# Kernel optimization log

Hardware: AMD Instinct MI355X
Metric: run time of the kernel (lower is better)

Reference implementation:

```python
import jax, jax.numpy as jnp
import numpy as np

EPS = 1e-6

def _ln(x, g, b):
    m = x.mean(-1, keepdims=True)
    v = jnp.var(x, axis=-1, keepdims=True)
    return (x - m) * jax.lax.rsqrt(v + EPS) * g + b

def _mha(x, qkv_w, out_w, out_b, heads, dh):
    # vit-style attention: Linear(dim, 3*heads*dh, bias=False), chunk into q,k,v
    B, N, _ = x.shape
    qkv = (x @ qkv_w).reshape(B, N, 3, heads, dh).transpose(2, 0, 3, 1, 4)
    q, k, v = qkv[0], qkv[1], qkv[2]                       # [B,H,N,dh]
    attn = jax.nn.softmax(jnp.einsum('bhid,bhjd->bhij', q, k) * (dh ** -0.5), axis=-1)
    o = jnp.einsum('bhij,bhjd->bhid', attn, v).transpose(0, 2, 1, 3).reshape(B, N, heads * dh)
    return o @ out_w + out_b

def _tx(x, p, heads, dh):
    # standard prenorm transformer stack, p = stacked per-layer params
    (l1g, l1b, qw, ow, ob, l2g, l2b, f1w, f1b, f2w, f2b, ng, nb) = p
    for i in range(l1g.shape[0]):
        x = x + _mha(_ln(x, l1g[i], l1b[i]), qw[i], ow[i], ob[i], heads, dh)
        h = _ln(x, l2g[i], l2b[i])
        x = x + jax.nn.gelu(h @ f1w[i] + f1b[i]) @ f2w[i] + f2b[i]
    return _ln(x, ng, nb)

def _ats(x, l1g, l1b, qkvw, qkvb, projw, projb, l2g, l2b, f1w, f1b, f2w, f2b):
    # ATS block: attention + CLS-significance-driven adaptive token resampling (gather)
    B, N, D = x.shape
    heads = 6
    dh = D // heads
    h = _ln(x, l1g, l1b)
    qkv = (h @ qkvw + qkvb).reshape(B, N, 3, heads, dh).transpose(2, 0, 3, 1, 4)
    q, k, v = qkv[0], qkv[1], qkv[2]
    attn = jax.nn.softmax(jnp.einsum('bhid,bhjd->bhij', q, k) * (dh ** -0.5), axis=-1)  # [B,H,N,N]
    y = jnp.einsum('bhij,bhjd->bhid', attn, v).transpose(0, 2, 1, 3).reshape(B, N, D)
    y = y @ projw + projb
    # significance score: cls attention * value norm (ATS, Fayyaz et al.)
    vn = jnp.linalg.norm(v, axis=-1)                        # [B,H,N]
    s = (attn[:, :, 0, 1:] * vn[:, :, 1:]).mean(axis=1)     # [B,N-1]
    s = s / (s.sum(-1, keepdims=True) + 1e-8)
    cdf = jnp.cumsum(s, axis=-1)                            # [B,N-1]
    # deterministic inverse-transform sampling of N-1 tokens
    u = (jnp.arange(N - 1, dtype=x.dtype) + 0.5) / (N - 1)
    idx = jax.vmap(lambda c: jnp.searchsorted(c, u))(cdf)
    idx = jnp.clip(idx, 0, N - 2) + 1                       # skip cls slot
    idx = jnp.concatenate([jnp.zeros((B, 1), idx.dtype), idx], axis=1)  # keep cls
    g = lambda a: jnp.take_along_axis(a, idx[:, :, None], axis=1)
    x = g(x) + g(y)
    h = _ln(x, l2g, l2b)
    return x + jax.nn.gelu(h @ f1w + f1b) @ f2w + f2b

def reference(x, patch_w, patch_b, pos_emb, space_token, temporal_token,
              s_ln1_g, s_ln1_b, s_qkv_w, s_out_w, s_out_b, s_ln2_g, s_ln2_b,
              s_fc1_w, s_fc1_b, s_fc2_w, s_fc2_b, s_norm_g, s_norm_b,
              t_ln1_g, t_ln1_b, t_qkv_w, t_out_w, t_out_b, t_ln2_g, t_ln2_b,
              t_fc1_w, t_fc1_b, t_fc2_w, t_fc2_b, t_norm_g, t_norm_b,
              a_ln1_g, a_ln1_b, a_qkv_w, a_qkv_b, a_proj_w, a_proj_b,
              a_ln2_g, a_ln2_b, a_fc1_w, a_fc1_b, a_fc2_w, a_fc2_b,
              final_g, final_b, h1_w, h1_b, h2_w, h2_b):
    B, T = x.shape[0], x.shape[1]
    BT, D, P, HP = B * T, 192, 16, 14
    # patch embedding (conv16s16 as unfold + linear), channel-major flattening
    xt = x.reshape(BT, 3, HP, P, HP, P).transpose(0, 2, 4, 1, 3, 5).reshape(BT, HP * HP, 3 * P * P)
    xt = (xt @ patch_w + patch_b).reshape(B, T, HP * HP, D)
    cls = jnp.broadcast_to(space_token.reshape(1, 1, 1, D), (B, T, 1, D))
    xt = jnp.concatenate([cls, xt], axis=2) + pos_emb      # [B,T,197,D]
    xt = xt.reshape(BT, 197, D)
    xt = _tx(xt, (s_ln1_g, s_ln1_b, s_qkv_w, s_out_w, s_out_b, s_ln2_g, s_ln2_b,
                  s_fc1_w, s_fc1_b, s_fc2_w, s_fc2_b, s_norm_g, s_norm_b), 6, 64)
    for i in range(a_ln1_g.shape[0]):
        xt = _ats(xt, a_ln1_g[i], a_ln1_b[i], a_qkv_w[i], a_qkv_b[i], a_proj_w[i],
                  a_proj_b[i], a_ln2_g[i], a_ln2_b[i], a_fc1_w[i], a_fc1_b[i],
                  a_fc2_w[i], a_fc2_b[i])
    xc = xt[:, 0].reshape(B, T, D)
    tt = jnp.broadcast_to(temporal_token, (B, 1, D))
    xc = jnp.concatenate([tt, xc], axis=1)                 # [B,T+1,D]
    xc = _tx(xc, (t_ln1_g, t_ln1_b, t_qkv_w, t_out_w, t_out_b, t_ln2_g, t_ln2_b,
                  t_fc1_w, t_fc1_b, t_fc2_w, t_fc2_b, t_norm_g, t_norm_b), 6, 64)
    f = jnp.max(xc, axis=1)                                # AdaptiveMaxPool1d(1) over tokens
    f = _ln(f, final_g, final_b)
    return jax.nn.relu(f @ h1_w + h1_b) @ h2_w + h2_b      # mlp_head -> [B,2]

def setup_inputs():
    key = jax.random.key(0)
    ks = iter(jax.random.split(key, 64))
    def rn(shape, s=0.02):
        return jax.random.normal(next(ks), shape, dtype=jnp.float32) * s
    d = {}
    d['x'] = jax.random.normal(next(ks), (16, 5, 3, 224, 224), dtype=jnp.float32)
    d['patch_w'] = rn((768, 192)); d['patch_b'] = jnp.zeros((192,), jnp.float32)
    d['pos_emb'] = rn((1, 5, 197, 192))
    d['space_token'] = rn((1, 1, 192)); d['temporal_token'] = rn((1, 1, 192))
    def tx(depth, n):
        d[n + '_ln1_g'] = jnp.ones((depth, 192), jnp.float32); d[n + '_ln1_b'] = jnp.zeros((depth, 192), jnp.float32)
        d[n + '_qkv_w'] = rn((depth, 192, 1152)); d[n + '_out_w'] = rn((depth, 384, 192)); d[n + '_out_b'] = jnp.zeros((depth, 192), jnp.float32)
        d[n + '_ln2_g'] = jnp.ones((depth, 192), jnp.float32); d[n + '_ln2_b'] = jnp.zeros((depth, 192), jnp.float32)
        d[n + '_fc1_w'] = rn((depth, 192, 768)); d[n + '_fc1_b'] = jnp.zeros((depth, 768), jnp.float32)
        d[n + '_fc2_w'] = rn((depth, 768, 192)); d[n + '_fc2_b'] = jnp.zeros((depth, 192), jnp.float32)
        d[n + '_norm_g'] = jnp.ones((192,), jnp.float32); d[n + '_norm_b'] = jnp.zeros((192,), jnp.float32)
    tx(2, 's'); tx(3, 't')
    d['a_ln1_g'] = jnp.ones((12, 192), jnp.float32); d['a_ln1_b'] = jnp.zeros((12, 192), jnp.float32)
    d['a_qkv_w'] = rn((12, 192, 576)); d['a_qkv_b'] = jnp.zeros((12, 576), jnp.float32)
    d['a_proj_w'] = rn((12, 192, 192)); d['a_proj_b'] = jnp.zeros((12, 192), jnp.float32)
    d['a_ln2_g'] = jnp.ones((12, 192), jnp.float32); d['a_ln2_b'] = jnp.zeros((12, 192), jnp.float32)
    d['a_fc1_w'] = rn((12, 192, 768)); d['a_fc1_b'] = jnp.zeros((12, 768), jnp.float32)
    d['a_fc2_w'] = rn((12, 768, 192)); d['a_fc2_b'] = jnp.zeros((12, 192), jnp.float32)
    d['final_g'] = jnp.ones((192,), jnp.float32); d['final_b'] = jnp.zeros((192,), jnp.float32)
    d['h1_w'] = rn((192, 64)); d['h1_b'] = jnp.zeros((64,), jnp.float32)
    d['h2_w'] = rn((64, 2)); d['h2_b'] = jnp.zeros((2,), jnp.float32)
    return d
```

## Files before the change

### kernel.cpp

```cpp
#include <hip/hip_runtime.h>
#include <hip/hip_bf16.h>
#include <math.h>

typedef float in_t;
typedef float out_t;

__device__ __forceinline__ float ldi(const in_t* p, size_t i) { return (float)p[i]; }

#define DMODEL 192
#define NTOK   197
#define BT_    80
#define ROWS_  (BT_*NTOK)

__device__ __forceinline__ float gelu_f(float v) {
  return 0.5f*v*(1.f + tanhf(0.7978845608028654f*(v + 0.044715f*v*v*v)));
}

__device__ __forceinline__ short f2bf(float f) {
  union { float f; unsigned u; } v; v.f = f;
  unsigned r = v.u + 0x7FFFu + ((v.u >> 16) & 1u);
  return (short)(r >> 16);
}

typedef __attribute__((ext_vector_type(8))) short bfrag;
typedef __attribute__((ext_vector_type(4))) float f32x4;

__global__ __launch_bounds__(256)
void wconv_k(const float* __restrict__ W, short* __restrict__ O, int K, int N)
{
  __shared__ float tile[32][33];
  const int l = blockIdx.z;
  const int k0 = blockIdx.y*32, n0 = blockIdx.x*32;
  const float* Wl = W + (size_t)l*K*N;
  short* Ol = O + (size_t)l*K*N;
  const int tx = threadIdx.x & 31, ty = threadIdx.x >> 5;
  #pragma unroll
  for (int r = ty; r < 32; r += 8) {
    int k = k0 + r, n = n0 + tx;
    tile[r][tx] = (k < K && n < N) ? Wl[(size_t)k*N + n] : 0.f;
  }
  __syncthreads();
  #pragma unroll
  for (int r = ty; r < 32; r += 8) {
    int n = n0 + r, k = k0 + tx;
    if (n < N && k < K) Ol[(size_t)n*K + k] = f2bf(tile[tx][r]);
  }
}

template<int EPI, int ABF, int OBF>
__global__ __launch_bounds__(256)
void gemmW_k(const void* __restrict__ Ain, const short* __restrict__ Wt,
             const float* __restrict__ bias, const float* __restrict__ R,
             void* __restrict__ Cout, float* __restrict__ Cout2,
             int M, int N, int K)
{
  constexpr int LP = 200;
  __shared__ short Asb[64][LP];
  __shared__ short Bsb[64][LP];
  const int t = threadIdx.x;
  const int w = t >> 6, lane = t & 63;
  const int bm0 = blockIdx.y*64, bn0 = blockIdx.x*64;
  const int sr = t >> 2;
  const int sk = (t & 3) * 8;
  f32x4 acc[4] = {};

  for (int k0 = 0; k0 < K; k0 += 192) {
    const int gm = bm0 + sr;
    #pragma unroll
    for (int cc = 0; cc < 6; ++cc) {
      const int kk = cc*32 + sk;
      short y[8] = {0,0,0,0,0,0,0,0};
      if (gm < M) {
        if (ABF == 0) {
          const float* ap = (const float*)Ain + (size_t)gm*K + k0 + kk;
          float4 v0 = *(const float4*)ap;
          float4 v1 = *(const float4*)(ap + 4);
          y[0]=f2bf(v0.x); y[1]=f2bf(v0.y); y[2]=f2bf(v0.z); y[3]=f2bf(v0.w);
          y[4]=f2bf(v1.x); y[5]=f2bf(v1.y); y[6]=f2bf(v1.z); y[7]=f2bf(v1.w);
        } else {
          *(bfrag*)y = *(const bfrag*)((const short*)Ain + (size_t)gm*K + k0 + kk);
        }
      }
      *(bfrag*)&Asb[sr][kk] = *(bfrag*)y;
      bfrag bv = *(const bfrag*)(Wt + (size_t)(bn0 + sr)*K + k0 + kk);
      *(bfrag*)&Bsb[sr][kk] = bv;
    }
    __syncthreads();
    const int fr = lane & 15, g8 = (lane >> 4) * 8;
    #pragma unroll
    for (int ks = 0; ks < 6; ++ks) {
      bfrag af = *(const bfrag*)&Asb[w*16 + fr][ks*32 + g8];
      #pragma unroll
      for (int nt = 0; nt < 4; ++nt) {
        bfrag bf = *(const bfrag*)&Bsb[nt*16 + fr][ks*32 + g8];
        acc[nt] = __builtin_amdgcn_mfma_f32_16x16x32_bf16(af, bf, acc[nt], 0, 0, 0);
      }
    }
    __syncthreads();
  }
  const int col = lane & 15, rg = (lane >> 4) * 4;
  #pragma unroll
  for (int nt = 0; nt < 4; ++nt) {
    int gn = bn0 + nt*16 + col;
    float bv = bias ? bias[gn] : 0.f;
    #pragma unroll
    for (int r = 0; r < 4; ++r) {
      int gm = bm0 + w*16 + rg + r;
      if (gm < M) {
        float v = acc[nt][r] + bv;
        if (EPI==1) v = gelu_f(v);
        if (EPI==2) v += R[(size_t)gm*N + gn];
        if (OBF==0)      ((float*)Cout)[(size_t)gm*N + gn] = v;
        else if (OBF==1) ((short*)Cout)[(size_t)gm*N + gn] = f2bf(v);
        else {
          if (gn < 384) ((short*)Cout)[(size_t)gm*384 + gn] = f2bf(v);
          else          Cout2[(size_t)gm*192 + (gn - 384)] = v;
        }
      }
    }
  }
}

__global__ __launch_bounds__(256)
void ffn_k(const float* __restrict__ Ain, const short* __restrict__ W1t,
           const float* __restrict__ b1, const short* __restrict__ W2t,
           const float* __restrict__ b2, const float* __restrict__ R,
           float* __restrict__ Cout, int M)
{
  constexpr int LP = 200, FP = 776;
  __shared__ short As[64][LP];
  __shared__ short Bs[64][LP];
  __shared__ short FF[64][FP];
  const int t = threadIdx.x;
  const int w = t >> 6, lane = t & 63;
  const int bm0 = blockIdx.x*64;
  const int sr = t >> 2;
  const int sk = (t & 3) * 8;
  const int fr = lane & 15, g8 = (lane >> 4) * 8;
  const int col = lane & 15, rg = (lane >> 4) * 4;

  {
    const int gm = bm0 + sr;
    #pragma unroll
    for (int cc = 0; cc < 6; ++cc) {
      const int kk = cc*32 + sk;
      short y[8] = {0,0,0,0,0,0,0,0};
      if (gm < M) {
        const float* ap = Ain + (size_t)gm*192 + kk;
        float4 v0 = *(const float4*)ap;
        float4 v1 = *(const float4*)(ap + 4);
        y[0]=f2bf(v0.x); y[1]=f2bf(v0.y); y[2]=f2bf(v0.z); y[3]=f2bf(v0.w);
        y[4]=f2bf(v1.x); y[5]=f2bf(v1.y); y[6]=f2bf(v1.z); y[7]=f2bf(v1.w);
      }
      *(bfrag*)&As[sr][kk] = *(bfrag*)y;
    }
  }
  for (int nc = 0; nc < 12; ++nc) {
    #pragma unroll
    for (int cc = 0; cc < 6; ++cc) {
      const int kk = cc*32 + sk;
      bfrag bv = *(const bfrag*)(W1t + (size_t)(nc*64 + sr)*192 + kk);
      *(bfrag*)&Bs[sr][kk] = bv;
    }
    __syncthreads();
    f32x4 acc[4] = {};
    #pragma unroll
    for (int ks = 0; ks < 6; ++ks) {
      bfrag af = *(const bfrag*)&As[w*16 + fr][ks*32 + g8];
      #pragma unroll
      for (int nt = 0; nt < 4; ++nt) {
        bfrag bf = *(const bfrag*)&Bs[nt*16 + fr][ks*32 + g8];
        acc[nt] = __builtin_amdgcn_mfma_f32_16x16x32_bf16(af, bf, acc[nt], 0, 0, 0);
      }
    }
    #pragma unroll
    for (int nt = 0; nt < 4; ++nt) {
      int gn = nc*64 + nt*16 + col;
      float bv = b1[gn];
      #pragma unroll
      for (int r = 0; r < 4; ++r)
        FF[w*16 + rg + r][gn] = f2bf(gelu_f(acc[nt][r] + bv));
    }
    __syncthreads();
  }
  for (int nc = 0; nc < 3; ++nc) {
    f32x4 acc[4] = {};
    for (int kc = 0; kc < 4; ++kc) {
      #pragma unroll
      for (int cc = 0; cc < 6; ++cc) {
        const int kk = cc*32 + sk;
        bfrag bv = *(const bfrag*)(W2t + (size_t)(nc*64 + sr)*768 + kc*192 + kk);
        *(bfrag*)&Bs[sr][kk] = bv;
      }
      __syncthreads();
      #pragma unroll
      for (int ks = 0; ks < 6; ++ks) {
        bfrag af = *(const bfrag*)&FF[w*16 + fr][kc*192 + ks*32 + g8];
        #pragma unroll
        for (int nt = 0; nt < 4; ++nt) {
          bfrag bf = *(const bfrag*)&Bs[nt*16 + fr][ks*32 + g8];
          acc[nt] = __builtin_amdgcn_mfma_f32_16x16x32_bf16(af, bf, acc[nt], 0, 0, 0);
        }
      }
      __syncthreads();
    }
    #pragma unroll
    for (int nt = 0; nt < 4; ++nt) {
      int gn = nc*64 + nt*16 + col;
      float bv = b2[gn];
      #pragma unroll
      for (int r = 0; r < 4; ++r) {
        int gm = bm0 + w*16 + rg + r;
        if (gm < M) {
          float v = acc[nt][r] + bv + R[(size_t)gm*192 + gn];
          Cout[(size_t)gm*192 + gn] = v;
        }
      }
    }
  }
}

__global__ __launch_bounds__(256)
void ln_k(const float* __restrict__ x, const in_t* __restrict__ g, const in_t* __restrict__ b,
          float* __restrict__ o, int rows)
{
  int t = threadIdx.x, wave = t>>6, lane = t&63;
  int r = blockIdx.x*4 + wave;
  if (r >= rows) return;
  const float* xr = x + (size_t)r*DMODEL;
  float e0 = xr[lane], e1 = xr[lane+64], e2 = xr[lane+128];
  float s = e0+e1+e2;
  #pragma unroll
  for (int off=32; off; off>>=1) s += __shfl_xor(s, off);
  float mean = s / 192.f;
  float d0=e0-mean, d1=e1-mean, d2=e2-mean;
  float v = d0*d0+d1*d1+d2*d2;
  #pragma unroll
  for (int off=32; off; off>>=1) v += __shfl_xor(v, off);
  float rs = 1.f / sqrtf(v/192.f + 1e-6f);
  float* orow = o + (size_t)r*DMODEL;
  orow[lane]     = d0*rs*ldi(g,lane)     + ldi(b,lane);
  orow[lane+64]  = d1*rs*ldi(g,lane+64)  + ldi(b,lane+64);
  orow[lane+128] = d2*rs*ldi(g,lane+128) + ldi(b,lane+128);
}

__global__ __launch_bounds__(256)
void gatherln_k(const float* __restrict__ X, const float* __restrict__ P,
                const int* __restrict__ idx, const in_t* __restrict__ g,
                const in_t* __restrict__ b, float* __restrict__ Xo,
                float* __restrict__ H2, int rows)
{
  int t = threadIdx.x, wave = t>>6, lane = t&63;
  int r = blockIdx.x*4 + wave;
  if (r >= rows) return;
  int bt = r / NTOK, n = r - bt*NTOK;
  int src = idx[(size_t)bt*NTOK + n];
  size_t sb = ((size_t)bt*NTOK + src)*DMODEL;
  float e0 = X[sb+lane]     + P[sb+lane];
  float e1 = X[sb+lane+64]  + P[sb+lane+64];
  float e2 = X[sb+lane+128] + P[sb+lane+128];
  float* xr = Xo + (size_t)r*DMODEL;
  xr[lane] = e0; xr[lane+64] = e1; xr[lane+128] = e2;
  float s = e0+e1+e2;
  #pragma unroll
  for (int off=32; off; off>>=1) s += __shfl_xor(s, off);
  float mean = s / 192.f;
  float d0=e0-mean, d1=e1-mean, d2=e2-mean;
  float v = d0*d0+d1*d1+d2*d2;
  #pragma unroll
  for (int off=32; off; off>>=1) v += __shfl_xor(v, off);
  float rs = 1.f / sqrtf(v/192.f + 1e-6f);
  float* orow = H2 + (size_t)r*DMODEL;
  orow[lane]     = d0*rs*ldi(g,lane)     + ldi(b,lane);
  orow[lane+64]  = d1*rs*ldi(g,lane+64)  + ldi(b,lane+64);
  orow[lane+128] = d2*rs*ldi(g,lane+128) + ldi(b,lane+128);
}

template<int DH, int W, int MODE>
__global__ __launch_bounds__(W*64)
void attnB_k(const short* __restrict__ qk, const float* __restrict__ vf,
             short* __restrict__ out, float* __restrict__ attn0,
             int heads, float scale)
{
  constexpr int NSEQ = 197;
  constexpr int NP   = 224;
  constexpr int KG   = DH/8;
  constexpr int CT   = DH/16;
  constexpr int NF   = DH/32;
  __shared__ short Kb[KG][NP][8];
  __shared__ short Vt[NP/8][DH][8];
  __shared__ short Ps[W][NP/8][16][8];

  const int bh = blockIdx.x;
  const int b = bh / heads, h = bh - b*heads;
  const int qks = ((MODE==1) ? 3 : 2)*heads*DH;
  const short* __restrict__ baseqk = qk + (size_t)b*NSEQ*qks;
  const int qo = h*DH, ko = heads*DH + h*DH;
  const int vs = heads*DH;
  const float* __restrict__ basev = (MODE==2) ? (vf + (size_t)b*NSEQ*vs) : nullptr;
  const int vo = (MODE==1) ? (2*heads*DH + h*DH) : (h*DH);
  const int t = threadIdx.x, w = t>>6, lane = t&63;

  {
    short z8[8] = {0,0,0,0,0,0,0,0};
    for (int idx = t; idx < NP*KG; idx += W*64) {
      int j = idx / KG, dg = idx - j*KG;
      bfrag kv = *(bfrag*)z8;
      if (j < NSEQ) kv = *(const bfrag*)(baseqk + (size_t)j*qks + ko + dg*8);
      *(bfrag*)&Kb[dg][j][0] = kv;
    }
  }
  for (int idx = t; idx < NP*DH; idx += W*64) {
    int j = idx / DH, d = idx - j*DH;
    short vv = 0;
    if (j < NSEQ) {
      if (MODE==1) vv = baseqk[(size_t)j*qks + vo + d];
      else         vv = f2bf(basev[(size_t)j*vs + vo + d]);
    }
    Vt[j>>3][d][j&7] = vv;
  }
  __syncthreads();

  const int c = lane & 15, g = lane >> 4, rg = g*4;
  const float NEG = -3.0e38f;

  for (int st = w; st < 13; st += W) {
    const int q0 = st*16;
    int qrow = q0 + c; if (qrow > NSEQ-1) qrow = NSEQ-1;
    bfrag aq[NF];
    {
      const short* qp = baseqk + (size_t)qrow*qks + qo + g*8;
      #pragma unroll
      for (int f = 0; f < NF; ++f) aq[f] = *(const bfrag*)(qp + f*32);
    }
    f32x4 sacc[14];
    #pragma unroll
    for (int jt = 0; jt < 14; ++jt) sacc[jt] = (f32x4){0.f,0.f,0.f,0.f};
    #pragma unroll
    for (int jt = 0; jt < 13; ++jt) {
      #pragma unroll
      for (int f = 0; f < NF; ++f) {
        bfrag bk = *(const bfrag*)&Kb[f*4 + g][jt*16 + c][0];
        sacc[jt] = __builtin_amdgcn_mfma_f32_16x16x32_bf16(aq[f], bk, sacc[jt], 0, 0, 0);
      }
    }
    float m0[4] = {NEG,NEG,NEG,NEG};
    #pragma unroll
    for (int jt = 0; jt < 14; ++jt) {
      const bool valid = (jt < 13) && (jt*16 + c < NSEQ);
      #pragma unroll
      for (int r = 0; r < 4; ++r) {
        float sv = valid ? sacc[jt][r]*scale : NEG;
        sacc[jt][r] = sv;
        m0[r] = fmaxf(m0[r], sv);
      }
    }
    #pragma unroll
    for (int off = 1; off < 16; off <<= 1)
      #pragma unroll
      for (int r = 0; r < 4; ++r) m0[r] = fmaxf(m0[r], __shfl_xor(m0[r], off));
    float sum[4] = {0.f,0.f,0.f,0.f};
    #pragma unroll
    for (int jt = 0; jt < 14; ++jt)
      #pragma unroll
      for (int r = 0; r < 4; ++r) {
        float e = expf(sacc[jt][r] - m0[r]);
        sacc[jt][r] = e;
        sum[r] += e;
      }
    #pragma unroll
    for (int off = 1; off < 16; off <<= 1)
      #pragma unroll
      for (int r = 0; r < 4; ++r) sum[r] += __shfl_xor(sum[r], off);
    float inv[4];
    #pragma unroll
    for (int r = 0; r < 4; ++r) inv[r] = 1.f / sum[r];

    if (attn0 != nullptr && st == 0 && g == 0) {
      #pragma unroll
      for (int jt = 0; jt < 13; ++jt) {
        int j = jt*16 + c;
        if (j < NSEQ) attn0[(size_t)bh*NSEQ + j] = sacc[jt][0]*inv[0];
      }
    }
    #pragma unroll
    for (int jt = 0; jt < 14; ++jt)
      #pragma unroll
      for (int r = 0; r < 4; ++r)
        Ps[w][jt*2 + (c>>3)][rg + r][c&7] = f2bf(sacc[jt][r]);
    f32x4 oacc[CT];
    #pragma unroll
    for (int ct = 0; ct < CT; ++ct) oacc[ct] = (f32x4){0.f,0.f,0.f,0.f};
    #pragma unroll
    for (int kc = 0; kc < 7; ++kc) {
      bfrag ap = *(const bfrag*)&Ps[w][kc*4 + g][c][0];
      #pragma unroll
      for (int ct = 0; ct < CT; ++ct) {
        bfrag bv = *(const bfrag*)&Vt[kc*4 + g][ct*16 + c][0];
        oacc[ct] = __builtin_amdgcn_mfma_f32_16x16x32_bf16(ap, bv, oacc[ct], 0, 0, 0);
      }
    }
    #pragma unroll
    for (int ct = 0; ct < CT; ++ct)
      #pragma unroll
      for (int r = 0; r < 4; ++r) {
        int q = q0 + rg + r;
        if (q < NSEQ)
          out[((size_t)b*NSEQ + q)*(size_t)(heads*DH) + h*DH + ct*16 + c] = f2bf(oacc[ct][r]*inv[r]);
      }
  }
}

template<int DH, int W>
__global__ __launch_bounds__(W*64)
void attn2r_k(const float* __restrict__ qkv, float* __restrict__ out,
              float* __restrict__ attn0, int Nseq, int heads, float scale)
{
  constexpr int QT = 8;
  constexpr int KTS = 204;
  constexpr int NPART = (DH == 64) ? 1 : 2;
  constexpr int DQ   = DH/4;
  constexpr int QPG  = 2;
  __shared__ float Kt[DH * KTS];
  __shared__ float Qt[W][DH][12];
  __shared__ float Ps[W][QT][200];

  const int bh = blockIdx.x;
  const int b = bh / heads, h = bh % heads;
  const int stride = 3 * heads * DH;
  const float* __restrict__ base = qkv + (size_t)b * Nseq * stride;
  const int qo = h * DH, ko = heads * DH + h * DH, vo = 2 * heads * DH + h * DH;
  const int t = threadIdx.x, w = t >> 6, lane = t & 63;

  for (int idx = t; idx < Nseq * DH; idx += W * 64) {
    int j = idx / DH, d0 = idx - j * DH;
    Kt[d0 * KTS + j] = base[(size_t)j * stride + ko + d0];
  }
  __syncthreads();

  const int d = lane & (DH - 1);
  const int nchunks = (Nseq + QT - 1) / QT;
  const int jcmax = (Nseq + 3) >> 2;
  const float NEG = -3.0e38f;
  const float4* Kt4 = (const float4*)Kt;

  const int part = (NPART == 2) ? (lane >> 5) : 0;
  const int qg   = (DH == 64) ? (lane >> 4) : ((lane >> 3) & 3);
  const int dq   = lane & (DQ - 1);
  const int dv   = 4 * dq;

  for (int ic = w; ic < nchunks; ic += W) {
    const int i0 = ic * QT;
    if ((DH == 64) || (lane >> 5) == 0) {
      #pragma unroll
      for (int q = 0; q < QT; ++q) {
        int i = i0 + q;
        Qt[w][d][q] = (i < Nseq) ? base[(size_t)i * stride + qo + d] : 0.f;
      }
    }
    float s[QT][4];
    #pragma unroll
    for (int q = 0; q < QT; ++q)
      #pragma unroll
      for (int u = 0; u < 4; ++u) s[q][u] = 0.f;
    #pragma unroll 4
    for (int dd = 0; dd < DH; ++dd) {
      float4 kv = (lane < 51) ? Kt4[dd * (KTS/4) + lane] : make_float4(0.f,0.f,0.f,0.f);
      float4 qA = *(const float4*)&Qt[w][dd][0];
      float4 qB = *(const float4*)&Qt[w][dd][4];
      float qv[8] = {qA.x, qA.y, qA.z, qA.w, qB.x, qB.y, qB.z, qB.w};
      float kr[4] = {kv.x, kv.y, kv.z, kv.w};
      #pragma unroll
      for (int q = 0; q < QT; ++q)
        #pragma unroll
        for (int u = 0; u < 4; ++u)
          s[q][u] = fmaf(qv[q], kr[u], s[q][u]);
    }
    float inv[QT];
    #pragma unroll
    for (int q = 0; q < QT; ++q) {
      float mx = NEG;
      #pragma unroll
      for (int u = 0; u < 4; ++u) {
        int j = 4*lane + u;
        s[q][u] = (j < Nseq) ? s[q][u]*scale : NEG;
        mx = fmaxf(mx, s[q][u]);
      }
      #pragma unroll
      for (int off = 32; off; off >>= 1) mx = fmaxf(mx, __shfl_xor(mx, off));
      float sum = 0.f;
      #pragma unroll
      for (int u = 0; u < 4; ++u) {
        float p = (4*lane + u < Nseq) ? expf(s[q][u] - mx) : 0.f;
        s[q][u] = p; sum += p;
      }
      #pragma unroll
      for (int off = 32; off; off >>= 1) sum += __shfl_xor(sum, off);
      inv[q] = 1.f / sum;
      if (lane < 50)
        *(float4*)&Ps[w][q][4*lane] = make_float4(s[q][0], s[q][1], s[q][2], s[q][3]);
    }
    if (attn0 != nullptr && i0 == 0) {
      #pragma unroll
      for (int u = 0; u < 4; ++u) {
        int j = 4*lane + u;
        if (j < Nseq) attn0[(size_t)bh*Nseq + j] = s[0][u]*inv[0];
      }
    }
    float o[QPG][4];
    #pragma unroll
    for (int qi = 0; qi < QPG; ++qi) { o[qi][0]=0.f; o[qi][1]=0.f; o[qi][2]=0.f; o[qi][3]=0.f; }
    const float* __restrict__ Vg = base + vo;
    for (int jc = part; jc < jcmax; jc += NPART) {
      const int jb = 4*jc;
      float4 V0 = make_float4(0.f,0.f,0.f,0.f), V1=V0, V2=V0, V3=V0;
      if (jb+0 < Nseq) V0 = *(const float4*)&Vg[(size_t)(jb+0)*stride + dv];
      if (jb+1 < Nseq) V1 = *(const float4*)&Vg[(size_t)(jb+1)*stride + dv];
      if (jb+2 < Nseq) V2 = *(const float4*)&Vg[(size_t)(jb+2)*stride + dv];
      if (jb+3 < Nseq) V3 = *(const float4*)&Vg[(size_t)(jb+3)*stride + dv];
      #pragma unroll
      for (int qi = 0; qi < QPG; ++qi) {
        float4 p4 = *(const float4*)&Ps[w][qg*QPG+qi][jb];
        o[qi][0] = fmaf(p4.w,V3.x, fmaf(p4.z,V2.x, fmaf(p4.y,V1.x, fmaf(p4.x,V0.x, o[qi][0]))));
        o[qi][1] = fmaf(p4.w,V3.y, fmaf(p4.z,V2.y, fmaf(p4.y,V1.y, fmaf(p4.x,V0.y, o[qi][1]))));
        o[qi][2] = fmaf(p4.w,V3.z, fmaf(p4.z,V2.z, fmaf(p4.y,V1.z, fmaf(p4.x,V0.z, o[qi][2]))));
        o[qi][3] = fmaf(p4.w,V3.w, fmaf(p4.z,V2.w, fmaf(p4.y,V1.w, fmaf(p4.x,V0.w, o[qi][3]))));
      }
    }
    if (NPART == 2) {
      #pragma unroll
      for (int qi = 0; qi < QPG; ++qi) {
        o[qi][0] += __shfl_xor(o[qi][0], 32);
        o[qi][1] += __shfl_xor(o[qi][1], 32);
        o[qi][2] += __shfl_xor(o[qi][2], 32);
        o[qi][3] += __shfl_xor(o[qi][3], 32);
      }
    }
    if (part == 0) {
      #pragma unroll
      for (int qi = 0; qi < QPG; ++qi) {
        float iv = inv[qi];
        if (qg == 1) iv = inv[QPG + qi];
        if (qg == 2) iv = inv[2*QPG + qi];
        if (qg == 3) iv = inv[3*QPG + qi];
        int i = i0 + qg*QPG + qi;
        if (i < Nseq) {
          float4 r = make_float4(o[qi][0]*iv, o[qi][1]*iv, o[qi][2]*iv, o[qi][3]*iv);
          *(float4*)&out[((size_t)b*Nseq + i)*(size_t)(heads*DH) + h*DH + dv] = r;
        }
      }
    }
  }
}

__global__ void patchify_k(const in_t* __restrict__ x, short* __restrict__ A)
{
  int idx = blockIdx.x*256 + threadIdx.x;
  const int total = BT_*196*768;
  if (idx >= total) return;
  int kc = idx % 768;
  int m  = idx / 768;
  int p  = m % 196;
  int bt = m / 196;
  int c  = kc >> 8;
  int py = (kc >> 4) & 15;
  int px = kc & 15;
  int ph = p / 14, pw = p % 14;
  size_t src = (((size_t)bt*3 + c)*224 + (ph*16+py))*224 + (pw*16+px);
  A[idx] = f2bf(ldi(x, src));
}

__global__ void assemble_k(const float* __restrict__ pt, const in_t* __restrict__ st,
                           const in_t* __restrict__ pe, float* __restrict__ X)
{
  int i = blockIdx.x*256 + threadIdx.x;
  const int total = BT_*NTOK*DMODEL;
  if (i >= total) return;
  int d  = i % DMODEL;
  int n  = (i / DMODEL) % NTOK;
  int bt = i / (DMODEL*NTOK);
  int tt = bt % 5;
  float base = (n == 0) ? ldi(st, d)
                        : pt[((size_t)bt*196 + (n-1))*DMODEL + d];
  X[i] = base + ldi(pe, ((size_t)tt*NTOK + n)*DMODEL + d);
}

__global__ __launch_bounds__(256)
void scoresample_k(const float* __restrict__ attn0, const float* __restrict__ Vf,
                   int* __restrict__ idxout)
{
  __shared__ float S[196];
  __shared__ float cdf[196];
  int b = blockIdx.x, t = threadIdx.x;
  if (t < 196) {
    int j = t + 1;
    float acc = 0.f;
    #pragma unroll
    for (int h = 0; h < 6; ++h) {
      float a0 = attn0[((size_t)b*6 + h)*NTOK + j];
      const float* v = Vf + ((size_t)b*NTOK + j)*192 + h*32;
      float ss = 0.f;
      #pragma unroll
      for (int d = 0; d < 32; ++d) ss += v[d]*v[d];
      acc += a0 * sqrtf(ss);
    }
    S[t] = acc / 6.0f;
  }
  __syncthreads();
  if (t == 0) {
    float tot = 0.f;
    for (int k = 0; k < 196; ++k) tot += S[k];
    float denom = tot + 1e-8f;
    float run = 0.f;
    for (int k = 0; k < 196; ++k) { run += S[k] / denom; cdf[k] = run; }
    idxout[(size_t)b*NTOK] = 0;
  }
  __syncthreads();
  if (t < 196) {
    float u = ((float)t + 0.5f) / 196.0f;
    int cnt = 0;
    for (int k = 0; k < 196; ++k) cnt += (cdf[k] < u) ? 1 : 0;
    int c = cnt > 195 ? 195 : cnt;
    idxout[(size_t)b*NTOK + 1 + t] = c + 1;
  }
}

__global__ void build_xc_k(const float* __restrict__ X, const in_t* __restrict__ tt,
                           float* __restrict__ xc)
{
  int i = blockIdx.x*256 + threadIdx.x;
  const int total = 16*6*DMODEL;
  if (i >= total) return;
  int d = i % DMODEL;
  int n = (i / DMODEL) % 6;
  int b = i / (DMODEL*6);
  xc[i] = (n == 0) ? ldi(tt, d)
                   : X[(((size_t)b*5 + (n-1))*NTOK + 0)*DMODEL + d];
}

__global__ __launch_bounds__(256)
void head_k(const float* __restrict__ xc, const in_t* __restrict__ fg, const in_t* __restrict__ fb,
            const in_t* __restrict__ w1, const in_t* __restrict__ b1,
            const in_t* __restrict__ w2, const in_t* __restrict__ b2,
            out_t* __restrict__ outp)
{
  __shared__ float fn[DMODEL];
  __shared__ float hid[64];
  __shared__ float mv[2];
  int b = blockIdx.x, t = threadIdx.x;
  if (t < DMODEL) {
    float m = xc[((size_t)b*6 + 0)*DMODEL + t];
    #pragma unroll
    for (int n = 1; n < 6; ++n) m = fmaxf(m, xc[((size_t)b*6 + n)*DMODEL + t]);
    fn[t] = m;
  }
  __syncthreads();
  if (t == 0) {
    float s = 0.f;
    for (int d = 0; d < DMODEL; ++d) s += fn[d];
    float mean = s / 192.f;
    float v = 0.f;
    for (int d = 0; d < DMODEL; ++d) { float dd = fn[d]-mean; v += dd*dd; }
    mv[0] = mean; mv[1] = 1.f / sqrtf(v/192.f + 1e-6f);
  }
  __syncthreads();
  if (t < DMODEL) fn[t] = (fn[t]-mv[0])*mv[1]*ldi(fg,t) + ldi(fb,t);
  __syncthreads();
  if (t < 64) {
    float a = ldi(b1, t);
    for (int d = 0; d < DMODEL; ++d) a += fn[d]*ldi(w1, (size_t)d*64 + t);
    hid[t] = fmaxf(a, 0.f);
  }
  __syncthreads();
  if (t < 2) {
    float a = ldi(b2, t);
    for (int j = 0; j < 64; ++j) a += hid[j]*ldi(w2, (size_t)j*2 + t);
    outp[(size_t)b*2 + t] = (out_t)a;
  }
}

extern "C" void kernel_launch(void* const* d_in, const int* in_sizes, int n_in,
                              void* d_out, int out_size, void* d_ws, size_t ws_size,
                              hipStream_t stream)
{
  if (n_in < 50) return;
  const in_t* x_in     = (const in_t*)d_in[0];
  const in_t* patch_w  = (const in_t*)d_in[1];
  const in_t* patch_b  = (const in_t*)d_in[2];
  const in_t* pos_emb  = (const in_t*)d_in[3];
  const in_t* space_tk = (const in_t*)d_in[4];
  const in_t* temp_tk  = (const in_t*)d_in[5];
  const in_t* s_ln1_g = (const in_t*)d_in[6];  const in_t* s_ln1_b = (const in_t*)d_in[7];
  const in_t* s_qkv_w = (const in_t*)d_in[8];  const in_t* s_out_w = (const in_t*)d_in[9];
  const in_t* s_out_b = (const in_t*)d_in[10]; const in_t* s_ln2_g = (const in_t*)d_in[11];
  const in_t* s_ln2_b = (const in_t*)d_in[12]; const in_t* s_fc1_w = (const in_t*)d_in[13];
  const in_t* s_fc1_b = (const in_t*)d_in[14]; const in_t* s_fc2_w = (const in_t*)d_in[15];
  const in_t* s_fc2_b = (const in_t*)d_in[16]; const in_t* s_nrm_g = (const in_t*)d_in[17];
  const in_t* s_nrm_b = (const in_t*)d_in[18];
  const in_t* t_ln1_g = (const in_t*)d_in[19]; const in_t* t_ln1_b = (const in_t*)d_in[20];
  const in_t* t_qkv_w = (const in_t*)d_in[21]; const in_t* t_out_w = (const in_t*)d_in[22];
  const in_t* t_out_b = (const in_t*)d_in[23]; const in_t* t_ln2_g = (const in_t*)d_in[24];
  const in_t* t_ln2_b = (const in_t*)d_in[25]; const in_t* t_fc1_w = (const in_t*)d_in[26];
  const in_t* t_fc1_b = (const in_t*)d_in[27]; const in_t* t_fc2_w = (const in_t*)d_in[28];
  const in_t* t_fc2_b = (const in_t*)d_in[29]; const in_t* t_nrm_g = (const in_t*)d_in[30];
  const in_t* t_nrm_b = (const in_t*)d_in[31];
  const in_t* a_ln1_g = (const in_t*)d_in[32]; const in_t* a_ln1_b = (const in_t*)d_in[33];
  const in_t* a_qkv_w = (const in_t*)d_in[34]; const in_t* a_qkv_b = (const in_t*)d_in[35];
  const in_t* a_prj_w = (const in_t*)d_in[36]; const in_t* a_prj_b = (const in_t*)d_in[37];
  const in_t* a_ln2_g = (const in_t*)d_in[38]; const in_t* a_ln2_b = (const in_t*)d_in[39];
  const in_t* a_fc1_w = (const in_t*)d_in[40]; const in_t* a_fc1_b = (const in_t*)d_in[41];
  const in_t* a_fc2_w = (const in_t*)d_in[42]; const in_t* a_fc2_b = (const in_t*)d_in[43];
  const in_t* final_g = (const in_t*)d_in[44]; const in_t* final_b = (const in_t*)d_in[45];
  const in_t* h1_w = (const in_t*)d_in[46];    const in_t* h1_b = (const in_t*)d_in[47];
  const in_t* h2_w = (const in_t*)d_in[48];    const in_t* h2_b = (const in_t*)d_in[49];

  float* ws = (float*)d_ws;
  size_t off = 0;
  auto alloc = [&](size_t nf) { size_t r = off; off += (nf + 63) & ~((size_t)63); return r; };
  size_t oX    = alloc((size_t)ROWS_*DMODEL);
  size_t oX2   = alloc((size_t)ROWS_*DMODEL);
  size_t oH    = alloc((size_t)ROWS_*DMODEL);
  size_t oH2   = alloc((size_t)ROWS_*DMODEL);
  size_t oY    = alloc((size_t)ROWS_*384);
  size_t oVf   = alloc((size_t)ROWS_*192);
  size_t oA0   = alloc((size_t)480*NTOK);
  size_t oXC   = alloc((size_t)16*6*DMODEL);
  size_t oIDX  = alloc((size_t)BT_*NTOK);
  size_t oQKVt = alloc((size_t)96*1152);
  size_t oFFt  = alloc((size_t)96*768);
  size_t oWB   = alloc((size_t)4202496 + 64);
  size_t oQKVb = alloc((size_t)ROWS_*1152/2 + 64);
  size_t oYb   = alloc((size_t)ROWS_*384/2 + 64);
  size_t oFFb  = alloc((size_t)ROWS_*768/2 + 64);
  if (ws_size < off*sizeof(float)) return;

  float* X    = ws + oX;
  float* X2   = ws + oX2;
  float* H    = ws + oH;
  float* H2   = ws + oH2;
  float* Y    = ws + oY;
  float* Vf   = ws + oVf;
  float* A0   = ws + oA0;
  float* XC   = ws + oXC;
  int*   IDX  = (int*)(ws + oIDX);
  float* QKVt = ws + oQKVt;
  float* FFt  = ws + oFFt;
  short* WB   = (short*)(ws + oWB);
  short* QKVb = (short*)(ws + oQKVb);
  short* Yb   = (short*)(ws + oYb);
  short* FFb  = (short*)(ws + oFFb);

  size_t wo = 0;
  auto wslot = [&](size_t n){ size_t r = wo; wo += n; return r; };
  size_t wPatch = wslot(147456);
  size_t wSqkv  = wslot(442368);
  size_t wSout  = wslot(147456);
  size_t wSfc1  = wslot(294912);
  size_t wSfc2  = wslot(294912);
  size_t wAqkv  = wslot(1327104);
  size_t wAprj  = wslot(442368);
  size_t wAfc1  = wslot(1769472);
  size_t wAfc2  = wslot(1769472);
  size_t wTqkv  = wslot(663552);
  size_t wTout  = wslot(221184);
  size_t wTfc1  = wslot(442368);
  size_t wTfc2  = wslot(442368);

  auto wconv = [&](const in_t* W, size_t slot, int K, int N, int L) {
    dim3 g(N/32, K/32, L);
    hipLaunchKernelGGL(wconv_k, g, dim3(256), 0, stream, W, WB + slot, K, N);
  };
  wconv(patch_w, wPatch, 768, 192, 1);
  wconv(s_qkv_w, wSqkv, 192, 1152, 2);
  wconv(s_out_w, wSout, 384, 192, 2);
  wconv(s_fc1_w, wSfc1, 192, 768, 2);
  wconv(s_fc2_w, wSfc2, 768, 192, 2);
  wconv(a_qkv_w, wAqkv, 192, 576, 12);
  wconv(a_prj_w, wAprj, 192, 192, 12);
  wconv(a_fc1_w, wAfc1, 192, 768, 12);
  wconv(a_fc2_w, wAfc2, 768, 192, 12);
  wconv(t_qkv_w, wTqkv, 192, 1152, 3);
  wconv(t_out_w, wTout, 384, 192, 3);
  wconv(t_fc1_w, wTfc1, 192, 768, 3);
  wconv(t_fc2_w, wTfc2, 768, 192, 3);

  auto gemm = [&](int epi, int abf, int obf, const void* A, const short* Wt,
                  const float* bias, const float* R, void* C, float* C2,
                  int M, int N, int K) {
    dim3 grid(N/64, (M+63)/64);
    if (obf==2)                        hipLaunchKernelGGL((gemmW_k<0,0,2>), grid, dim3(256), 0, stream, A, Wt, bias, R, C, C2, M, N, K);
    else if (epi==0 && abf==0 && obf==0) hipLaunchKernelGGL((gemmW_k<0,0,0>), grid, dim3(256), 0, stream, A, Wt, bias, R, C, C2, M, N, K);
    else if (epi==0 && abf==0 && obf==1) hipLaunchKernelGGL((gemmW_k<0,0,1>), grid, dim3(256), 0, stream, A, Wt, bias, R, C, C2, M, N, K);
    else if (epi==0 && abf==1 && obf==0) hipLaunchKernelGGL((gemmW_k<0,1,0>), grid, dim3(256), 0, stream, A, Wt, bias, R, C, C2, M, N, K);
    else if (epi==1 && obf==1)         hipLaunchKernelGGL((gemmW_k<1,0,1>), grid, dim3(256), 0, stream, A, Wt, bias, R, C, C2, M, N, K);
    else if (epi==1)                   hipLaunchKernelGGL((gemmW_k<1,0,0>), grid, dim3(256), 0, stream, A, Wt, bias, R, C, C2, M, N, K);
    else if (epi==2 && abf==1)         hipLaunchKernelGGL((gemmW_k<2,1,0>), grid, dim3(256), 0, stream, A, Wt, bias, R, C, C2, M, N, K);
    else                               hipLaunchKernelGGL((gemmW_k<2,0,0>), grid, dim3(256), 0, stream, A, Wt, bias, R, C, C2, M, N, K);
  };
  auto ln = [&](const float* xi, const in_t* g, const in_t* b, float* o, int rows) {
    hipLaunchKernelGGL(ln_k, dim3((rows+3)/4), dim3(256), 0, stream, xi, g, b, o, rows);
  };
  auto ffn = [&](const float* A, size_t w1, const float* b1, size_t w2, const float* b2,
                 const float* R, float* C, int M) {
    hipLaunchKernelGGL(ffn_k, dim3((M+63)/64), dim3(256), 0, stream,
                       A, WB + w1, b1, WB + w2, b2, R, C, M);
  };

  {
    int total = BT_*196*768;
    hipLaunchKernelGGL(patchify_k, dim3((total+255)/256), dim3(256), 0, stream, x_in, FFb);
    gemm(0, 1, 0, FFb, WB + wPatch, patch_b, nullptr, Y, nullptr, 15680, 192, 768);
    int tot2 = BT_*NTOK*DMODEL;
    hipLaunchKernelGGL(assemble_k, dim3((tot2+255)/256), dim3(256), 0, stream, Y, space_tk, pos_emb, X);
  }

  const float sc64 = 0.125f;
  const float sc32 = 0.17677669529663687f;

  for (int i = 0; i < 2; ++i) {
    ln(X, s_ln1_g + (size_t)i*192, s_ln1_b + (size_t)i*192, H, ROWS_);
    gemm(0, 0, 1, H, WB + wSqkv + (size_t)i*192*1152, nullptr, nullptr, QKVb, nullptr, ROWS_, 1152, 192);
    hipLaunchKernelGGL((attnB_k<64,8,1>), dim3(BT_*6), dim3(512), 0, stream, QKVb, (const float*)nullptr, Yb, (float*)nullptr, 6, sc64);
    gemm(2, 1, 0, Yb, WB + wSout + (size_t)i*384*192, s_out_b + (size_t)i*192, X, X, nullptr, ROWS_, 192, 384);
    ln(X, s_ln2_g + (size_t)i*192, s_ln2_b + (size_t)i*192, H, ROWS_);
    ffn(H, wSfc1 + (size_t)i*192*768, s_fc1_b + (size_t)i*768,
        wSfc2 + (size_t)i*768*192, s_fc2_b + (size_t)i*192, X, X, ROWS_);
  }
  ln(X, s_nrm_g, s_nrm_b, X, ROWS_);

  float* xa = X; float* xb = X2;
  for (int i = 0; i < 12; ++i) {
    ln(xa, a_ln1_g + (size_t)i*192, a_ln1_b + (size_t)i*192, H, ROWS_);
    gemm(0, 0, 2, H, WB + wAqkv + (size_t)i*192*576, a_qkv_b + (size_t)i*576, nullptr, QKVb, Vf, ROWS_, 576, 192);
    hipLaunchKernelGGL((attnB_k<32,4,2>), dim3(BT_*6), dim3(256), 0, stream, QKVb, Vf, Yb, A0, 6, sc32);
    gemm(0, 1, 0, Yb, WB + wAprj + (size_t)i*192*192, a_prj_b + (size_t)i*192, nullptr, H, nullptr, ROWS_, 192, 192);
    hipLaunchKernelGGL(scoresample_k, dim3(BT_), dim3(256), 0, stream, A0, Vf, IDX);
    hipLaunchKernelGGL(gatherln_k, dim3((ROWS_+3)/4), dim3(256), 0, stream,
                       xa, H, IDX, a_ln2_g + (size_t)i*192, a_ln2_b + (size_t)i*192, xb, H2, ROWS_);
    ffn(H2, wAfc1 + (size_t)i*192*768, a_fc1_b + (size_t)i*768,
        wAfc2 + (size_t)i*768*192, a_fc2_b + (size_t)i*192, xb, xb, ROWS_);
    float* tmp = xa; xa = xb; xb = tmp;
  }

  {
    int tot = 16*6*DMODEL;
    hipLaunchKernelGGL(build_xc_k, dim3((tot+255)/256), dim3(256), 0, stream, xa, temp_tk, XC);
  }
  const int MT = 16*6;
  for (int i = 0; i < 3; ++i) {
    ln(XC, t_ln1_g + (size_t)i*192, t_ln1_b + (size_t)i*192, H, MT);
    gemm(0, 0, 0, H, WB + wTqkv + (size_t)i*192*1152, nullptr, nullptr, QKVt, nullptr, MT, 1152, 192);
    hipLaunchKernelGGL((attn2r_k<64,8>), dim3(16*6), dim3(512), 0, stream, QKVt, Y, (float*)nullptr, 6, 6, sc64);
    gemm(2, 0, 0, Y, WB + wTout + (size_t)i*384*192, t_out_b + (size_t)i*192, XC, XC, nullptr, MT, 192, 384);
    ln(XC, t_ln2_g + (size_t)i*192, t_ln2_b + (size_t)i*192, H, MT);
    gemm(1, 0, 0, H, WB + wTfc1 + (size_t)i*192*768, t_fc1_b + (size_t)i*768, nullptr, FFt, nullptr, MT, 768, 192);
    gemm(2, 0, 0, FFt, WB + wTfc2 + (size_t)i*768*192, t_fc2_b + (size_t)i*192, XC, XC, nullptr, MT, 192, 768);
  }
  ln(XC, t_nrm_g, t_nrm_b, XC, MT);

  hipLaunchKernelGGL(head_k, dim3(16), dim3(256), 0, stream, XC, final_g, final_b,
                     h1_w, h1_b, h2_w, h2_b, (out_t*)d_out);
}
```

Before: 2.663 ms.

## Stream FFN weights from global and split hidden buffer to cut LDS

The fused FFN kernel no longer stages weight tiles in shared memory. Each wave loads W1/W2 fragments directly from global memory and works only on its own 16 rows, which removes most block barriers. The GELU hidden buffer is processed in two halves, with fc2 partial sums kept in 12 register accumulators, roughly halving LDS use so more blocks can be resident. The trade-offs are uncoalesced, cache-dependent global weight loads per MFMA and higher register pressure.

```diff
diff --git a/kernel.cpp b/kernel.cpp
--- a/kernel.cpp
+++ b/kernel.cpp
@@ -127,10 +127,8 @@
            const float* __restrict__ b2, const float* __restrict__ R,
            float* __restrict__ Cout, int M)
 {
-  constexpr int LP = 200, FP = 776;
-  __shared__ short As[64][LP];
-  __shared__ short Bs[64][LP];
-  __shared__ short FF[64][FP];
+  __shared__ short As[64][200];
+  __shared__ short FF[64][392];
   const int t = threadIdx.x;
   const int w = t >> 6, lane = t & 63;
   const int bm0 = blockIdx.x*64;
@@ -138,6 +136,7 @@
   const int sk = (t & 3) * 8;
   const int fr = lane & 15, g8 = (lane >> 4) * 8;
   const int col = lane & 15, rg = (lane >> 4) * 4;
+  const int row = w*16 + fr;
 
   {
     const int gm = bm0 + sr;
@@ -155,66 +154,56 @@
       *(bfrag*)&As[sr][kk] = *(bfrag*)y;
     }
   }
-  for (int nc = 0; nc < 12; ++nc) {
-    #pragma unroll
-    for (int cc = 0; cc < 6; ++cc) {
-      const int kk = cc*32 + sk;
-      bfrag bv = *(const bfrag*)(W1t + (size_t)(nc*64 + sr)*192 + kk);
-      *(bfrag*)&Bs[sr][kk] = bv;
-    }
-    __syncthreads();
-    f32x4 acc[4] = {};
-    #pragma unroll
-    for (int ks = 0; ks < 6; ++ks) {
-      bfrag af = *(const bfrag*)&As[w*16 + fr][ks*32 + g8];
-      #pragma unroll
-      for (int nt = 0; nt < 4; ++nt) {
-        bfrag bf = *(const bfrag*)&Bs[nt*16 + fr][ks*32 + g8];
-        acc[nt] = __builtin_amdgcn_mfma_f32_16x16x32_bf16(af, bf, acc[nt], 0, 0, 0);
-      }
-    }
-    #pragma unroll
-    for (int nt = 0; nt < 4; ++nt) {
-      int gn = nc*64 + nt*16 + col;
-      float bv = b1[gn];
-      #pragma unroll
-      for (int r = 0; r < 4; ++r)
-        FF[w*16 + rg + r][gn] = f2bf(gelu_f(acc[nt][r] + bv));
-    }
-    __syncthreads();
-  }
-  for (int nc = 0; nc < 3; ++nc) {
-    f32x4 acc[4] = {};
-    for (int kc = 0; kc < 4; ++kc) {
-      #pragma unroll
-      for (int cc = 0; cc < 6; ++cc) {
-        const int kk = cc*32 + sk;
-        bfrag bv = *(const bfrag*)(W2t + (size_t)(nc*64 + sr)*768 + kc*192 + kk);
-        *(bfrag*)&Bs[sr][kk] = bv;
-      }
-      __syncthreads();
+  __syncthreads();
+
+  f32x4 acc2[12] = {};
+
+  #pragma unroll
+  for (int half = 0; half < 2; ++half) {
+    for (int nc6 = 0; nc6 < 6; ++nc6) {
+      const int nc = half*6 + nc6;
+      f32x4 a1[4] = {};
       #pragma unroll
       for (int ks = 0; ks < 6; ++ks) {
-        bfrag af = *(const bfrag*)&FF[w*16 + fr][kc*192 + ks*32 + g8];
+        bfrag af = *(const bfrag*)&As[row][ks*32 + g8];
         #pragma unroll
         for (int nt = 0; nt < 4; ++nt) {
-          bfrag bf = *(const bfrag*)&Bs[nt*16 + fr][ks*32 + g8];
-          acc[nt] = __builtin_amdgcn_mfma_f32_16x16x32_bf16(af, bf, acc[nt], 0, 0, 0);
+          bfrag bf = *(const bfrag*)(W1t + (size_t)(nc*64 + nt*16 + fr)*192 + ks*32 + g8);
+          a1[nt] = __builtin_amdgcn_mfma_f32_16x16x32_bf16(af, bf, a1[nt], 0, 0, 0);
         }
       }
-      __syncthreads();
-    }
-    #pragma unroll
-    for (int nt = 0; nt < 4; ++nt) {
-      int gn = nc*64 + nt*16 + col;
-      float bv = b2[gn];
-      #pragma unroll
-      for (int r = 0; r < 4; ++r) {
-        int gm = bm0 + w*16 + rg + r;
-        if (gm < M) {
-          float v = acc[nt][r] + bv + R[(size_t)gm*192 + gn];
-          Cout[(size_t)gm*192 + gn] = v;
+      #pragma unroll
+      for (int nt = 0; nt < 4; ++nt) {
+        int gn = nc*64 + nt*16 + col;
+        float bv = b1[gn];
+        #pragma unroll
+        for (int r = 0; r < 4; ++r)
+          FF[w*16 + rg + r][nc6*64 + nt*16 + col] = f2bf(gelu_f(a1[nt][r] + bv));
+      }
+    }
+    #pragma unroll
+    for (int kcl = 0; kcl < 2; ++kcl) {
+      #pragma unroll
+      for (int ks = 0; ks < 6; ++ks) {
+        bfrag af = *(const bfrag*)&FF[row][kcl*192 + ks*32 + g8];
+        #pragma unroll
+        for (int nt = 0; nt < 12; ++nt) {
+          bfrag bf = *(const bfrag*)(W2t + (size_t)(nt*16 + fr)*768 + (half*2 + kcl)*192 + ks*32 + g8);
+          acc2[nt] = __builtin_amdgcn_mfma_f32_16x16x32_bf16(af, bf, acc2[nt], 0, 0, 0);
         }
+      }
+    }
+  }
+  #pragma unroll
+  for (int nt = 0; nt < 12; ++nt) {
+    int gn = nt*16 + col;
+    float bv = b2[gn];
+    #pragma unroll
+    for (int r = 0; r < 4; ++r) {
+      int gm = bm0 + w*16 + rg + r;
+      if (gm < M) {
+        float v = acc2[nt][r] + bv + R[(size_t)gm*192 + gn];
+        Cout[(size_t)gm*192 + gn] = v;
       }
     }
   }
```

Measured after the change: 3.416 ms. 28.2% more time.

## Use 8 waves in fused FFN kernel, splitting N tiles across wave pairs

Applied to the files above, without the earlier changes.

The fused FFN kernel goes from 4 to 8 waves per block. Each row band of 16 is now shared by two waves that each compute half of the 64-column tile. The second GEMM loop is reordered to keep all 6 output accumulators live across the K chunks, so the FF tile is reused. A missing barrier after the A-tile staging is also added. The aim is more latency hiding and more MFMA parallelism per block, at the cost of more threads contending for the same LDS and barriers.

```diff
diff --git a/kernel.cpp b/kernel.cpp
--- a/kernel.cpp
+++ b/kernel.cpp
@@ -121,29 +121,30 @@
   }
 }
 
-__global__ __launch_bounds__(256)
+__global__ __launch_bounds__(512)
 void ffn_k(const float* __restrict__ Ain, const short* __restrict__ W1t,
            const float* __restrict__ b1, const short* __restrict__ W2t,
            const float* __restrict__ b2, const float* __restrict__ R,
            float* __restrict__ Cout, int M)
 {
-  constexpr int LP = 200, FP = 776;
-  __shared__ short As[64][LP];
-  __shared__ short Bs[64][LP];
-  __shared__ short FF[64][FP];
+  __shared__ short As[64][200];
+  __shared__ short Bs[64][200];
+  __shared__ short FF[64][776];
   const int t = threadIdx.x;
   const int w = t >> 6, lane = t & 63;
   const int bm0 = blockIdx.x*64;
-  const int sr = t >> 2;
-  const int sk = (t & 3) * 8;
+  const int sr = t >> 3;
+  const int sk8 = (t & 7) * 8;
   const int fr = lane & 15, g8 = (lane >> 4) * 8;
   const int col = lane & 15, rg = (lane >> 4) * 4;
+  const int band = w & 3, nh = w >> 2;
+  const int row = band*16 + fr;
 
   {
     const int gm = bm0 + sr;
     #pragma unroll
-    for (int cc = 0; cc < 6; ++cc) {
-      const int kk = cc*32 + sk;
+    for (int cc = 0; cc < 3; ++cc) {
+      const int kk = cc*64 + sk8;
       short y[8] = {0,0,0,0,0,0,0,0};
       if (gm < M) {
         const float* ap = Ain + (size_t)gm*192 + kk;
@@ -155,64 +156,70 @@
       *(bfrag*)&As[sr][kk] = *(bfrag*)y;
     }
   }
+  __syncthreads();
+
   for (int nc = 0; nc < 12; ++nc) {
     #pragma unroll
-    for (int cc = 0; cc < 6; ++cc) {
-      const int kk = cc*32 + sk;
+    for (int cc = 0; cc < 3; ++cc) {
+      const int kk = cc*64 + sk8;
       bfrag bv = *(const bfrag*)(W1t + (size_t)(nc*64 + sr)*192 + kk);
       *(bfrag*)&Bs[sr][kk] = bv;
     }
     __syncthreads();
-    f32x4 acc[4] = {};
+    f32x4 a1[2] = {};
     #pragma unroll
     for (int ks = 0; ks < 6; ++ks) {
-      bfrag af = *(const bfrag*)&As[w*16 + fr][ks*32 + g8];
-      #pragma unroll
-      for (int nt = 0; nt < 4; ++nt) {
-        bfrag bf = *(const bfrag*)&Bs[nt*16 + fr][ks*32 + g8];
-        acc[nt] = __builtin_amdgcn_mfma_f32_16x16x32_bf16(af, bf, acc[nt], 0, 0, 0);
-      }
-    }
-    #pragma unroll
-    for (int nt = 0; nt < 4; ++nt) {
-      int gn = nc*64 + nt*16 + col;
+      bfrag af = *(const bfrag*)&As[row][ks*32 + g8];
+      #pragma unroll
+      for (int ntl = 0; ntl < 2; ++ntl) {
+        bfrag bf = *(const bfrag*)&Bs[(nh*2+ntl)*16 + fr][ks*32 + g8];
+        a1[ntl] = __builtin_amdgcn_mfma_f32_16x16x32_bf16(af, bf, a1[ntl], 0, 0, 0);
+      }
+    }
+    #pragma unroll
+    for (int ntl = 0; ntl < 2; ++ntl) {
+      int gn = nc*64 + (nh*2+ntl)*16 + col;
       float bv = b1[gn];
       #pragma unroll
       for (int r = 0; r < 4; ++r)
-        FF[w*16 + rg + r][gn] = f2bf(gelu_f(acc[nt][r] + bv));
+        FF[band*16 + rg + r][gn] = f2bf(gelu_f(a1[ntl][r] + bv));
     }
     __syncthreads();
   }
-  for (int nc = 0; nc < 3; ++nc) {
-    f32x4 acc[4] = {};
-    for (int kc = 0; kc < 4; ++kc) {
-      #pragma unroll
-      for (int cc = 0; cc < 6; ++cc) {
-        const int kk = cc*32 + sk;
+
+  f32x4 acc2[6] = {};
+  for (int kc = 0; kc < 4; ++kc) {
+    for (int nc = 0; nc < 3; ++nc) {
+      #pragma unroll
+      for (int cc = 0; cc < 3; ++cc) {
+        const int kk = cc*64 + sk8;
         bfrag bv = *(const bfrag*)(W2t + (size_t)(nc*64 + sr)*768 + kc*192 + kk);
         *(bfrag*)&Bs[sr][kk] = bv;
       }
       __syncthreads();
       #pragma unroll
       for (int ks = 0; ks < 6; ++ks) {
-        bfrag af = *(const bfrag*)&FF[w*16 + fr][kc*192 + ks*32 + g8];
+        bfrag af = *(const bfrag*)&FF[row][kc*192 + ks*32 + g8];
         #pragma unroll
-        for (int nt = 0; nt < 4; ++nt) {
-          bfrag bf = *(const bfrag*)&Bs[nt*16 + fr][ks*32 + g8];
-          acc[nt] = __builtin_amdgcn_mfma_f32_16x16x32_bf16(af, bf, acc[nt], 0, 0, 0);
+        for (int ntl = 0; ntl < 2; ++ntl) {
+          bfrag bf = *(const bfrag*)&Bs[(nh*2+ntl)*16 + fr][ks*32 + g8];
+          acc2[nc*2+ntl] = __builtin_amdgcn_mfma_f32_16x16x32_bf16(af, bf, acc2[nc*2+ntl], 0, 0, 0);
         }
       }
       __syncthreads();
     }
-    #pragma unroll
-    for (int nt = 0; nt < 4; ++nt) {
-      int gn = nc*64 + nt*16 + col;
+  }
+  #pragma unroll
+  for (int nc = 0; nc < 3; ++nc) {
+    #pragma unroll
+    for (int ntl = 0; ntl < 2; ++ntl) {
+      int gn = (nc*4 + nh*2 + ntl)*16 + col;
       float bv = b2[gn];
       #pragma unroll
       for (int r = 0; r < 4; ++r) {
-        int gm = bm0 + w*16 + rg + r;
+        int gm = bm0 + band*16 + rg + r;
         if (gm < M) {
-          float v = acc[nt][r] + bv + R[(size_t)gm*192 + gn];
+          float v = acc2[nc*2+ntl][r] + bv + R[(size_t)gm*192 + gn];
           Cout[(size_t)gm*192 + gn] = v;
         }
       }
@@ -802,7 +809,7 @@
   };
   auto ffn = [&](const float* A, size_t w1, const float* b1, size_t w2, const float* b2,
                  const float* R, float* C, int M) {
-    hipLaunchKernelGGL(ffn_k, dim3((M+63)/64), dim3(256), 0, stream,
+    hipLaunchKernelGGL(ffn_k, dim3((M+63)/64), dim3(512), 0, stream,
                        A, WB + w1, b1, WB + w2, b2, R, C, M);
   };
 
```

Measured after the change: 2.478 ms (median of 2 runs). 1.07x faster.
